# Kernel optimization log

Hardware: AMD Instinct MI355X
Metric: run time of the kernel (lower is better)

The kernel has to match this reference:

```python
import jax, jax.numpy as jnp
import numpy as np

N_NODES = 100000
N_EDGES = 1600000
EMB = 128
N_LAYERS = 3
BN_EPS = 1e-5


def setup_inputs() -> dict:
    key = jax.random.key(0)
    k1, k2, k3 = jax.random.split(key, 3)
    feats = jax.random.normal(k1, (N_NODES, EMB), dtype=jnp.float32)
    edge_index = jax.random.randint(k2, (2, N_EDGES), 0, N_NODES, dtype=jnp.int64)
    # Glorot-ish scaled weights per layer
    W = jax.random.normal(k3, (N_LAYERS, EMB, EMB), dtype=jnp.float32) * (1.0 / np.sqrt(EMB))
    b = jnp.zeros((N_LAYERS, EMB), dtype=jnp.float32)
    gamma = jnp.ones((N_LAYERS, EMB), dtype=jnp.float32)
    beta = jnp.zeros((N_LAYERS, EMB), dtype=jnp.float32)
    return {"feats": feats, "edge_index": edge_index, "W": W, "b": b, "gamma": gamma, "beta": beta}


def _gcn_layer(h, row, col, W_l, b_l):
    # GCNConv (add_self_loops=False, normalize=True): x = h @ W, symmetric-norm scatter-add, + bias
    x = h @ W_l  # [N, D]
    ones = jnp.ones((row.shape[0],), dtype=h.dtype)
    deg = jax.ops.segment_sum(ones, col, num_segments=N_NODES)  # in-degree of targets
    dinv = jnp.where(deg > 0, jax.lax.rsqrt(jnp.maximum(deg, 1.0)), 0.0)
    norm = dinv[row] * dinv[col]  # [E]
    msg = x[row] * norm[:, None]  # gather + scale, [E, D]
    out = jax.ops.segment_sum(msg, col, num_segments=N_NODES)  # scatter-add
    return out + b_l


def _batch_norm(h, gamma_l, beta_l):
    mu = jnp.mean(h, axis=0)
    var = jnp.mean(jnp.square(h - mu), axis=0)  # biased var (torch BN training math)
    return (h - mu) * jax.lax.rsqrt(var + BN_EPS) * gamma_l + beta_l


def reference(feats, edge_index, W, b, gamma, beta):
    row, col = edge_index[0], edge_index[1]  # source, target
    h = feats
    for l in range(N_LAYERS):
        h = _gcn_layer(h, row, col, W[l], b[l])
        h = _batch_norm(h, gamma[l], beta[l])
        # dropout treated as identity (eval mode); residual=False; JK='last'
    return h
```

## Files before the change

### kernel.cpp

```cpp
#include <hip/hip_runtime.h>
#include <cstdint>
#include <cstddef>

#define BN_EPS 1e-5f
#define NCHUNK 256

typedef short bf16x8 __attribute__((ext_vector_type(8)));
typedef float f32x4 __attribute__((ext_vector_type(4)));


__device__ __forceinline__ int edge_at(const void* e, long long i, int m64) {
  return m64 ? (int)((const long long*)e)[i] : ((const int*)e)[i];
}

__device__ __forceinline__ unsigned short f2bf(float f) {
  unsigned int u = __float_as_uint(f);
  unsigned int r = (u + 0x7FFFu + ((u >> 16) & 1u)) >> 16;
  return (unsigned short)r;
}

__device__ __forceinline__ unsigned int pack2bf(float lo, float hi) {
  return (unsigned int)f2bf(lo) | ((unsigned int)f2bf(hi) << 16);
}

__global__ void detect_kernel(const int* __restrict__ e, int* __restrict__ mode) {
  int nz = 0;
  for (int i = 1; i < 512; i += 2) nz |= e[i];
  mode[0] = (nz == 0) ? 1 : 0;
}


__global__ __launch_bounds__(256) void count_kernel(const void* __restrict__ edges,
                                                    const int* __restrict__ mode,
                                                    int* __restrict__ blockcounts,
                                                    int E, int nb, int chunk) {
  __shared__ int h[1024];
  int m = mode[0];
  for (int i = threadIdx.x; i < nb; i += 256) h[i] = 0;
  __syncthreads();
  long long lo = (long long)blockIdx.x * chunk;
  long long hi = lo + chunk;
  if (hi > E) hi = E;
  for (long long i = lo + threadIdx.x; i < hi; i += 256) {
    int c = edge_at(edges, (long long)E + i, m);
    atomicAdd(&h[c >> 8], 1);
  }
  __syncthreads();
  for (int j = threadIdx.x; j < nb; j += 256)
    blockcounts[(size_t)j * NCHUNK + blockIdx.x] = h[j];
}

__global__ __launch_bounds__(256) void scan1_kernel(const int* __restrict__ src,
                                                    int* __restrict__ tprefix,
                                                    int* __restrict__ bsum, int n) {
  __shared__ int s[256];
  int t = threadIdx.x;
  int gid = blockIdx.x * 256 + t;
  int base = gid * 4;
  int sum = 0;
#pragma unroll
  for (int j = 0; j < 4; j++) {
    int i = base + j;
    if (i < n) sum += src[i];
  }
  s[t] = sum;
  __syncthreads();
  for (int off = 1; off < 256; off <<= 1) {
    int v = (t >= off) ? s[t - off] : 0;
    __syncthreads();
    s[t] += v;
    __syncthreads();
  }
  tprefix[gid] = s[t] - sum;
  if (t == 255) bsum[blockIdx.x] = s[255];
}

__global__ __launch_bounds__(256) void scan2_kernel(int* __restrict__ bsum, int nbk,
                                                    int* __restrict__ out, int n) {
  __shared__ int s[256];
  int t = threadIdx.x;
  int v = (t < nbk) ? bsum[t] : 0;
  s[t] = v;
  __syncthreads();
  for (int off = 1; off < 256; off <<= 1) {
    int u = (t >= off) ? s[t - off] : 0;
    __syncthreads();
    s[t] += u;
    __syncthreads();
  }
  if (t < nbk) bsum[t] = s[t] - v;
  if (t == 255) out[n] = s[255];
}

__global__ __launch_bounds__(256) void scan3_kernel(const int* __restrict__ src,
                                                    const int* __restrict__ tprefix,
                                                    const int* __restrict__ bsum,
                                                    int* __restrict__ out, int n) {
  int gid = blockIdx.x * 256 + threadIdx.x;
  int run = bsum[blockIdx.x] + tprefix[gid];
  int base = gid * 4;
#pragma unroll
  for (int j = 0; j < 4; j++) {
    int i = base + j;
    if (i < n) {
      int c = src[i];
      out[i] = run;
      run += c;
    }
  }
}

__global__ __launch_bounds__(256) void scatter_kernel(const void* __restrict__ edges,
                                                      const int* __restrict__ mode,
                                                      const int* __restrict__ moff,
                                                      int* __restrict__ pairs,
                                                      int E, int nb, int chunk) {
  __shared__ int cur[1024];
  int m = mode[0];
  for (int j = threadIdx.x; j < nb; j += 256)
    cur[j] = moff[(size_t)j * NCHUNK + blockIdx.x];
  __syncthreads();
  long long lo = (long long)blockIdx.x * chunk;
  long long hi = lo + chunk;
  if (hi > E) hi = E;
  for (long long i = lo + threadIdx.x; i < hi; i += 256) {
    int r = edge_at(edges, i, m);
    int c = edge_at(edges, (long long)E + i, m);
    int pos = atomicAdd(&cur[c >> 8], 1);
    pairs[pos] = (r << 8) | (c & 255);
  }
}

__global__ __launch_bounds__(256) void passB12_kernel(const int* __restrict__ pairs,
                                                      const int* __restrict__ moff,
                                                      float* __restrict__ dinv,
                                                      int* __restrict__ offsets,
                                                      int* __restrict__ csr_row, int n) {
  __shared__ int h[256];
  __shared__ int s[256];
  int t = threadIdx.x;
  int b = blockIdx.x;
  h[t] = 0;
  __syncthreads();
  int lo = moff[(size_t)b * NCHUNK];
  int hi = moff[(size_t)(b + 1) * NCHUNK];
  for (int e = lo + t; e < hi; e += 256)
    atomicAdd(&h[pairs[e] & 255], 1);
  __syncthreads();
  int d = h[t];
  s[t] = d;
  __syncthreads();
  for (int off = 1; off < 256; off <<= 1) {
    int v = (t >= off) ? s[t - off] : 0;
    __syncthreads();
    s[t] += v;
    __syncthreads();
  }
  int start = lo + s[t] - d;
  int node = b * 256 + t;
  if (node < n) {
    offsets[node] = start;
    dinv[node] = d > 0 ? rsqrtf((float)d) : 0.f;
    if (node == n - 1) offsets[n] = hi;
  }
  s[t] = start;
  __syncthreads();
  for (int e = lo + t; e < hi; e += 256) {
    int p = pairs[e];
    int pos = atomicAdd(&s[p & 255], 1);
    csr_row[pos] = p >> 8;
  }
}

__global__ __launch_bounds__(256) void prepWR_kernel(const float* __restrict__ W,
                                                     const float* __restrict__ colstats,
                                                     const float* __restrict__ gamma,
                                                     const float* __restrict__ beta,
                                                     float invN, int use_affine,
                                                     unsigned short* __restrict__ Wt,
                                                     float* __restrict__ rbias) {
  __shared__ float sc[128], sh[128];
  int t = threadIdx.x;
  if (t < 128) {
    float scv = 1.f, shv = 0.f;
    if (use_affine) {
      float mu = colstats[t] * invN;
      float var = colstats[128 + t] * invN - mu * mu;
      var = fmaxf(var, 0.f);
      scv = gamma[t] * rsqrtf(var + BN_EPS);
      shv = beta[t] - mu * scv;
    }
    sc[t] = scv;
    sh[t] = shv;
  }
  __syncthreads();
  int idx = blockIdx.x * 256 + t;
  int nc = idx >> 7, k = idx & 127;
  Wt[(size_t)nc * 128 + k] = f2bf(W[(size_t)k * 128 + nc] * sc[k]);
  if (blockIdx.x == 0 && t < 128) {
    float s = 0.f;
    if (use_affine) {
      for (int kk = 0; kk < 128; kk++) s += sh[kk] * W[(size_t)kk * 128 + t];
    }
    rbias[t] = s;
  }
}

template <int A_IS_FP32>
__global__ __launch_bounds__(256) void gemm_mfma_kernel(
    const void* __restrict__ Ain, const unsigned short* __restrict__ Wt,
    const float* __restrict__ rbias, const float* __restrict__ dinv,
    unsigned short* __restrict__ xb, int n) {
  int l = threadIdx.x & 63;
  int w = threadIdx.x >> 6;
  int row0 = blockIdx.x * 64 + w * 16;
  int am = row0 + (l & 15);
  int amc = am < n ? am : n - 1;
  int kg = l >> 4;

  f32x4 acc[8];
#pragma unroll
  for (int nt = 0; nt < 8; nt++) {
    f32x4 zv = {0.f, 0.f, 0.f, 0.f};
    acc[nt] = zv;
  }

#pragma unroll
  for (int kk = 0; kk < 4; kk++) {
    bf16x8 a;
    if (A_IS_FP32) {
      const float* ap = (const float*)Ain + (size_t)amc * 128 + kk * 32 + kg * 8;
      float4 f0 = *(const float4*)ap;
      float4 f1 = *(const float4*)(ap + 4);
      a[0] = (short)f2bf(f0.x); a[1] = (short)f2bf(f0.y);
      a[2] = (short)f2bf(f0.z); a[3] = (short)f2bf(f0.w);
      a[4] = (short)f2bf(f1.x); a[5] = (short)f2bf(f1.y);
      a[6] = (short)f2bf(f1.z); a[7] = (short)f2bf(f1.w);
    } else {
      a = *(const bf16x8*)((const unsigned short*)Ain + (size_t)amc * 128 + kk * 32 + kg * 8);
    }
#pragma unroll
    for (int nt = 0; nt < 8; nt++) {
      bf16x8 b = *(const bf16x8*)(Wt + (size_t)(nt * 16 + (l & 15)) * 128 + kk * 32 + kg * 8);
      acc[nt] = __builtin_amdgcn_mfma_f32_16x16x32_bf16(a, b, acc[nt], 0, 0, 0);
    }
  }

  int col0 = l & 15;
  int rbase = row0 + (l >> 4) * 4;
  float dv[4];
#pragma unroll
  for (int r = 0; r < 4; r++) {
    int rr = rbase + r;
    dv[r] = dinv[rr < n ? rr : n - 1];
  }
#pragma unroll
  for (int nt = 0; nt < 8; nt++) {
    float rb = rbias[nt * 16 + col0];
#pragma unroll
    for (int r = 0; r < 4; r++) {
      int rr = rbase + r;
      if (rr < n)
        xb[(size_t)rr * 128 + nt * 16 + col0] = f2bf((acc[nt][r] + rb) * dv[r]);
    }
  }
}

template <int F32OUT>
__global__ __launch_bounds__(256, 4) void agg_kernel(
    const uint4* __restrict__ x4, const int* __restrict__ csr_row,
    const int* __restrict__ offsets, const float* __restrict__ dinv,
    void* __restrict__ z, int n) {
  int node = blockIdx.x * 16 + (threadIdx.x >> 4);
  int d8 = threadIdx.x & 15;
  if (node >= n) return;
  int lo = offsets[node], hi = offsets[node + 1];
  float a0[8] = {}, a1[8] = {}, a2[8] = {}, a3[8] = {};
#define ACC8(A, v)                                                         \
  A[0] += __uint_as_float((v).x << 16); A[1] += __uint_as_float((v).x & 0xffff0000u); \
  A[2] += __uint_as_float((v).y << 16); A[3] += __uint_as_float((v).y & 0xffff0000u); \
  A[4] += __uint_as_float((v).z << 16); A[5] += __uint_as_float((v).z & 0xffff0000u); \
  A[6] += __uint_as_float((v).w << 16); A[7] += __uint_as_float((v).w & 0xffff0000u);
  int e = lo;
  for (; e + 8 <= hi; e += 8) {
    int r0 = csr_row[e];
    int r1 = csr_row[e + 1];
    int r2 = csr_row[e + 2];
    int r3 = csr_row[e + 3];
    int r4 = csr_row[e + 4];
    int r5 = csr_row[e + 5];
    int r6 = csr_row[e + 6];
    int r7 = csr_row[e + 7];
    uint4 v0 = x4[(size_t)r0 * 16 + d8];
    uint4 v1 = x4[(size_t)r1 * 16 + d8];
    uint4 v2 = x4[(size_t)r2 * 16 + d8];
    uint4 v3 = x4[(size_t)r3 * 16 + d8];
    uint4 v4 = x4[(size_t)r4 * 16 + d8];
    uint4 v5 = x4[(size_t)r5 * 16 + d8];
    uint4 v6 = x4[(size_t)r6 * 16 + d8];
    uint4 v7 = x4[(size_t)r7 * 16 + d8];
    ACC8(a0, v0) ACC8(a1, v1) ACC8(a2, v2) ACC8(a3, v3)
    ACC8(a0, v4) ACC8(a1, v5) ACC8(a2, v6) ACC8(a3, v7)
  }
  for (; e + 4 <= hi; e += 4) {
    int r0 = csr_row[e];
    int r1 = csr_row[e + 1];
    int r2 = csr_row[e + 2];
    int r3 = csr_row[e + 3];
    uint4 v0 = x4[(size_t)r0 * 16 + d8];
    uint4 v1 = x4[(size_t)r1 * 16 + d8];
    uint4 v2 = x4[(size_t)r2 * 16 + d8];
    uint4 v3 = x4[(size_t)r3 * 16 + d8];
    ACC8(a0, v0) ACC8(a1, v1) ACC8(a2, v2) ACC8(a3, v3)
  }
  for (; e < hi; e++) {
    uint4 v = x4[(size_t)csr_row[e] * 16 + d8];
    ACC8(a0, v)
  }
#undef ACC8
  float dvn = dinv[node];
  float s[8];
#pragma unroll
  for (int j = 0; j < 8; j++) s[j] = (a0[j] + a1[j] + a2[j] + a3[j]) * dvn;
  if (F32OUT) {
    float* zp = (float*)z + (size_t)node * 128 + d8 * 8;
    *(float4*)zp = make_float4(s[0], s[1], s[2], s[3]);
    *(float4*)(zp + 4) = make_float4(s[4], s[5], s[6], s[7]);
  } else {
    uint4 o = make_uint4(pack2bf(s[0], s[1]), pack2bf(s[2], s[3]),
                         pack2bf(s[4], s[5]), pack2bf(s[6], s[7]));
    *(uint4*)((unsigned short*)z + (size_t)node * 128 + d8 * 8) = o;
  }
}

template <int F32IN>
__global__ __launch_bounds__(256) void stats2_kernel(
    const void* __restrict__ z, float* __restrict__ partial, int total8) {
  __shared__ float ps[256];
  int t = threadIdx.x;
  ps[t] = 0.f;
  __syncthreads();
  int d8 = t & 15;
  float s[8] = {}, q[8] = {};
  int idx = blockIdx.x * 256 + t;
  int stride = gridDim.x * 256;
  for (int i = idx; i < total8; i += stride) {
    float v[8];
    if (F32IN) {
      const float* zp = (const float*)z + (size_t)i * 8;
      float4 f0 = *(const float4*)zp;
      float4 f1 = *(const float4*)(zp + 4);
      v[0] = f0.x; v[1] = f0.y; v[2] = f0.z; v[3] = f0.w;
      v[4] = f1.x; v[5] = f1.y; v[6] = f1.z; v[7] = f1.w;
    } else {
      uint4 u = ((const uint4*)z)[i];
      v[0] = __uint_as_float(u.x << 16); v[1] = __uint_as_float(u.x & 0xffff0000u);
      v[2] = __uint_as_float(u.y << 16); v[3] = __uint_as_float(u.y & 0xffff0000u);
      v[4] = __uint_as_float(u.z << 16); v[5] = __uint_as_float(u.z & 0xffff0000u);
      v[6] = __uint_as_float(u.w << 16); v[7] = __uint_as_float(u.w & 0xffff0000u);
    }
#pragma unroll
    for (int j = 0; j < 8; j++) { s[j] += v[j]; q[j] += v[j] * v[j]; }
  }
#pragma unroll
  for (int j = 0; j < 8; j++) {
    atomicAdd(&ps[d8 * 8 + j], s[j]);
    atomicAdd(&ps[128 + d8 * 8 + j], q[j]);
  }
  __syncthreads();
  partial[(size_t)blockIdx.x * 256 + t] = ps[t];
}

__global__ __launch_bounds__(256) void reduce_stats_kernel(
    const float* __restrict__ partial, float* __restrict__ out, int nblk) {
  __shared__ float red[256];
  int c = blockIdx.x;
  float s = 0.f;
  for (int i = threadIdx.x; i < nblk; i += 256) s += partial[(size_t)i * 256 + c];
  red[threadIdx.x] = s;
  __syncthreads();
  for (int o = 128; o > 0; o >>= 1) {
    if (threadIdx.x < o) red[threadIdx.x] += red[threadIdx.x + o];
    __syncthreads();
  }
  if (threadIdx.x == 0) out[c] = red[0];
}

__global__ __launch_bounds__(256) void norm_kernel(
    float* __restrict__ z, const float* __restrict__ colstats,
    const float* __restrict__ gamma, const float* __restrict__ beta,
    float invN, int total4) {
  __shared__ float sc[128], sh[128];
  int t = threadIdx.x;
  if (t < 128) {
    float mu = colstats[t] * invN;
    float var = colstats[128 + t] * invN - mu * mu;
    var = fmaxf(var, 0.f);
    float s = gamma[t] * rsqrtf(var + BN_EPS);
    sc[t] = s;
    sh[t] = beta[t] - mu * s;
  }
  __syncthreads();
  int idx = blockIdx.x * blockDim.x + t;
  int stride = gridDim.x * blockDim.x;
  for (int i = idx; i < total4; i += stride) {
    float4 v = ((const float4*)z)[i];
    int d0 = (i & 31) * 4;
    v.x = v.x * sc[d0] + sh[d0];
    v.y = v.y * sc[d0 + 1] + sh[d0 + 1];
    v.z = v.z * sc[d0 + 2] + sh[d0 + 2];
    v.w = v.w * sc[d0 + 3] + sh[d0 + 3];
    ((float4*)z)[i] = v;
  }
}


extern "C" void kernel_launch(void* const* d_in, const int* in_sizes, int n_in,
                              void* d_out, int out_size, void* d_ws, size_t ws_size,
                              hipStream_t stream) {
  const float* feats = (const float*)d_in[0];
  const void* edges = d_in[1];
  const float* W = (const float*)d_in[2];
  const float* gamma = (const float*)d_in[4];
  const float* beta = (const float*)d_in[5];

  const int n = in_sizes[0] / 128;
  const int E = in_sizes[1] / 2;

  const int nb = (n + 255) / 256;
  const int m = nb * NCHUNK;
  const int chunk = (E + NCHUNK - 1) / NCHUNK;
  const int sb_m = (m + 1023) / 1024;
  const int nagg = (n + 15) / 16;
  const int nstat = 1024;

  char* ws = (char*)d_ws;
  size_t off = 0;
  unsigned short* xb = (unsigned short*)(ws + off); off += (size_t)n * 128 * 2; off = (off + 255) & ~(size_t)255;
  float* dinv = (float*)(ws + off); off += (size_t)n * 4;
  int* offsets = (int*)(ws + off); off += (size_t)(n + 1) * 4; off = (off + 255) & ~(size_t)255;
  int* csr_row = (int*)(ws + off); off += (size_t)E * 4; off = (off + 255) & ~(size_t)255;
  int* pairs = (int*)(ws + off); off += (size_t)E * 4; off = (off + 255) & ~(size_t)255;
  int* blockcounts = (int*)(ws + off); off += (size_t)m * 4; off = (off + 255) & ~(size_t)255;
  int* moff = (int*)(ws + off); off += (size_t)(m + 1) * 4; off = (off + 255) & ~(size_t)255;
  int* tprefix = (int*)(ws + off); off += (size_t)sb_m * 256 * 4; off = (off + 255) & ~(size_t)255;
  int* bsum = (int*)(ws + off); off += 256 * 4;
  unsigned short* Wt = (unsigned short*)(ws + off); off += 128 * 128 * 2; off = (off + 255) & ~(size_t)255;
  float* rbias = (float*)(ws + off); off += 128 * 4;
  float* colstats = (float*)(ws + off); off += 256 * 4;
  int* mode = (int*)(ws + off); off += 4;

  float* partial = (float*)pairs;

  detect_kernel<<<1, 1, 0, stream>>>((const int*)edges, mode);
  count_kernel<<<NCHUNK, 256, 0, stream>>>(edges, mode, blockcounts, E, nb, chunk);
  scan1_kernel<<<sb_m, 256, 0, stream>>>(blockcounts, tprefix, bsum, m);
  scan2_kernel<<<1, 256, 0, stream>>>(bsum, sb_m, moff, m);
  scan3_kernel<<<sb_m, 256, 0, stream>>>(blockcounts, tprefix, bsum, moff, m);
  scatter_kernel<<<NCHUNK, 256, 0, stream>>>(edges, mode, moff, pairs, E, nb, chunk);
  passB12_kernel<<<nb, 256, 0, stream>>>(pairs, moff, dinv, offsets, csr_row, n);

  unsigned short* zb = (unsigned short*)d_out;
  float* zf = (float*)d_out;
  const int ggrid = (n + 63) / 64;
  const int total8 = n * 16;
  const float invN = 1.0f / (float)n;

  for (int l = 0; l < 3; l++) {
    prepWR_kernel<<<64, 256, 0, stream>>>(W + (size_t)l * 16384, colstats,
                                          gamma + l * 128, beta + l * 128, invN,
                                          l > 0 ? 1 : 0, Wt, rbias);
    if (l == 0)
      gemm_mfma_kernel<1><<<ggrid, 256, 0, stream>>>(feats, Wt, rbias, dinv, xb, n);
    else
      gemm_mfma_kernel<0><<<ggrid, 256, 0, stream>>>(zb, Wt, rbias, dinv, xb, n);
    if (l < 2) {
      agg_kernel<0><<<nagg, 256, 0, stream>>>(
          (const uint4*)xb, csr_row, offsets, dinv, zb, n);
      stats2_kernel<0><<<nstat, 256, 0, stream>>>(zb, partial, total8);
    } else {
      agg_kernel<1><<<nagg, 256, 0, stream>>>(
          (const uint4*)xb, csr_row, offsets, dinv, zf, n);
      stats2_kernel<1><<<nstat, 256, 0, stream>>>(zf, partial, total8);
    }
    reduce_stats_kernel<<<256, 256, 0, stream>>>(partial, colstats, nstat);
  }
  norm_kernel<<<2048, 256, 0, stream>>>(zf, colstats, gamma + 2 * 128, beta + 2 * 128,
                                        invN, (n * 128) / 4);
}
```

Measured before the change: 485.1 us.

## Stage weights in LDS, swap MFMA operands for packed stores, drop 8-wide agg unroll

The GEMM kernel now copies the transposed bf16 weight matrix into padded shared memory once per block and reads B fragments from LDS instead of global memory. It swaps the MFMA operand roles so each lane owns one output row with four consecutive columns, which allows packed 8-byte bf16 stores and a single dinv load per lane. Separately, the aggregation kernel loses its occupancy hint and its 8-edge unrolled loop, leaving the 4-edge loop. The LDS staging costs about 34KB and a block-wide barrier per GEMM block, and the aggregation change reduces memory-level parallelism in exchange for fewer registers.

```diff
diff --git a/kernel.cpp b/kernel.cpp
--- a/kernel.cpp
+++ b/kernel.cpp
@@ -4,6 +4,7 @@
 
 #define BN_EPS 1e-5f
 #define NCHUNK 256
+#define WT_PITCH 136
 
 typedef short bf16x8 __attribute__((ext_vector_type(8)));
 typedef float f32x4 __attribute__((ext_vector_type(4)));
@@ -211,12 +212,41 @@
     const void* __restrict__ Ain, const unsigned short* __restrict__ Wt,
     const float* __restrict__ rbias, const float* __restrict__ dinv,
     unsigned short* __restrict__ xb, int n) {
-  int l = threadIdx.x & 63;
-  int w = threadIdx.x >> 6;
+  __shared__ unsigned short wt[128 * WT_PITCH];
+  int t = threadIdx.x;
+  {
+    int row = t >> 1, half = t & 1;
+    const uint4* src = (const uint4*)(Wt + (size_t)row * 128 + half * 64);
+    uint4* dst = (uint4*)(wt + row * WT_PITCH + half * 64);
+#pragma unroll
+    for (int j = 0; j < 8; j++) dst[j] = src[j];
+  }
+  __syncthreads();
+
+  int l = t & 63;
+  int w = t >> 6;
   int row0 = blockIdx.x * 64 + w * 16;
-  int am = row0 + (l & 15);
-  int amc = am < n ? am : n - 1;
+  int m = row0 + (l & 15);
+  int mc = m < n ? m : n - 1;
   int kg = l >> 4;
+
+  bf16x8 b[4];
+#pragma unroll
+  for (int kk = 0; kk < 4; kk++) {
+    if (A_IS_FP32) {
+      const float* ap = (const float*)Ain + (size_t)mc * 128 + kk * 32 + kg * 8;
+      float4 f0 = *(const float4*)ap;
+      float4 f1 = *(const float4*)(ap + 4);
+      bf16x8 bb;
+      bb[0] = (short)f2bf(f0.x); bb[1] = (short)f2bf(f0.y);
+      bb[2] = (short)f2bf(f0.z); bb[3] = (short)f2bf(f0.w);
+      bb[4] = (short)f2bf(f1.x); bb[5] = (short)f2bf(f1.y);
+      bb[6] = (short)f2bf(f1.z); bb[7] = (short)f2bf(f1.w);
+      b[kk] = bb;
+    } else {
+      b[kk] = *(const bf16x8*)((const unsigned short*)Ain + (size_t)mc * 128 + kk * 32 + kg * 8);
+    }
+  }
 
   f32x4 acc[8];
 #pragma unroll
@@ -227,47 +257,28 @@
 
 #pragma unroll
   for (int kk = 0; kk < 4; kk++) {
-    bf16x8 a;
-    if (A_IS_FP32) {
-      const float* ap = (const float*)Ain + (size_t)amc * 128 + kk * 32 + kg * 8;
-      float4 f0 = *(const float4*)ap;
-      float4 f1 = *(const float4*)(ap + 4);
-      a[0] = (short)f2bf(f0.x); a[1] = (short)f2bf(f0.y);
-      a[2] = (short)f2bf(f0.z); a[3] = (short)f2bf(f0.w);
-      a[4] = (short)f2bf(f1.x); a[5] = (short)f2bf(f1.y);
-      a[6] = (short)f2bf(f1.z); a[7] = (short)f2bf(f1.w);
-    } else {
-      a = *(const bf16x8*)((const unsigned short*)Ain + (size_t)amc * 128 + kk * 32 + kg * 8);
-    }
 #pragma unroll
     for (int nt = 0; nt < 8; nt++) {
-      bf16x8 b = *(const bf16x8*)(Wt + (size_t)(nt * 16 + (l & 15)) * 128 + kk * 32 + kg * 8);
-      acc[nt] = __builtin_amdgcn_mfma_f32_16x16x32_bf16(a, b, acc[nt], 0, 0, 0);
-    }
-  }
-
-  int col0 = l & 15;
-  int rbase = row0 + (l >> 4) * 4;
-  float dv[4];
-#pragma unroll
-  for (int r = 0; r < 4; r++) {
-    int rr = rbase + r;
-    dv[r] = dinv[rr < n ? rr : n - 1];
-  }
+      bf16x8 a = *(const bf16x8*)(wt + (size_t)(nt * 16 + (l & 15)) * WT_PITCH + kk * 32 + kg * 8);
+      acc[nt] = __builtin_amdgcn_mfma_f32_16x16x32_bf16(a, b[kk], acc[nt], 0, 0, 0);
+    }
+  }
+
+  float dv = dinv[mc];
+  int colbase = kg * 4;
 #pragma unroll
   for (int nt = 0; nt < 8; nt++) {
-    float rb = rbias[nt * 16 + col0];
-#pragma unroll
-    for (int r = 0; r < 4; r++) {
-      int rr = rbase + r;
-      if (rr < n)
-        xb[(size_t)rr * 128 + nt * 16 + col0] = f2bf((acc[nt][r] + rb) * dv[r]);
-    }
+    int c0 = nt * 16 + colbase;
+    float4 rb = *(const float4*)&rbias[c0];
+    unsigned int w0 = pack2bf((acc[nt][0] + rb.x) * dv, (acc[nt][1] + rb.y) * dv);
+    unsigned int w1 = pack2bf((acc[nt][2] + rb.z) * dv, (acc[nt][3] + rb.w) * dv);
+    if (m < n)
+      *(uint2*)(xb + (size_t)m * 128 + c0) = make_uint2(w0, w1);
   }
 }
 
 template <int F32OUT>
-__global__ __launch_bounds__(256, 4) void agg_kernel(
+__global__ __launch_bounds__(256) void agg_kernel(
     const uint4* __restrict__ x4, const int* __restrict__ csr_row,
     const int* __restrict__ offsets, const float* __restrict__ dinv,
     void* __restrict__ z, int n) {
@@ -282,26 +293,6 @@
   A[4] += __uint_as_float((v).z << 16); A[5] += __uint_as_float((v).z & 0xffff0000u); \
   A[6] += __uint_as_float((v).w << 16); A[7] += __uint_as_float((v).w & 0xffff0000u);
   int e = lo;
-  for (; e + 8 <= hi; e += 8) {
-    int r0 = csr_row[e];
-    int r1 = csr_row[e + 1];
-    int r2 = csr_row[e + 2];
-    int r3 = csr_row[e + 3];
-    int r4 = csr_row[e + 4];
-    int r5 = csr_row[e + 5];
-    int r6 = csr_row[e + 6];
-    int r7 = csr_row[e + 7];
-    uint4 v0 = x4[(size_t)r0 * 16 + d8];
-    uint4 v1 = x4[(size_t)r1 * 16 + d8];
-    uint4 v2 = x4[(size_t)r2 * 16 + d8];
-    uint4 v3 = x4[(size_t)r3 * 16 + d8];
-    uint4 v4 = x4[(size_t)r4 * 16 + d8];
-    uint4 v5 = x4[(size_t)r5 * 16 + d8];
-    uint4 v6 = x4[(size_t)r6 * 16 + d8];
-    uint4 v7 = x4[(size_t)r7 * 16 + d8];
-    ACC8(a0, v0) ACC8(a1, v1) ACC8(a2, v2) ACC8(a3, v3)
-    ACC8(a0, v4) ACC8(a1, v5) ACC8(a2, v6) ACC8(a3, v7)
-  }
   for (; e + 4 <= hi; e += 4) {
     int r0 = csr_row[e];
     int r1 = csr_row[e + 1];
```

Result: faster. 422.9 us (-12.8%).
